# Performance work log

Measured on AMD Instinct MI355X. Metric: run time of the kernel, lower is better.

Reference implementation:

```python
import jax, jax.numpy as jnp
import numpy as np

D_MODEL = 1024
NUM_HEADS = 16
D_K = D_MODEL // NUM_HEADS
D_FF = 4096
B, S = 4, 2048
EPS = 1e-5


def _linear_params(key, d_in, d_out):
    # torch nn.Linear default init: U(-1/sqrt(d_in), 1/sqrt(d_in))
    k1, k2 = jax.random.split(key)
    bound = 1.0 / np.sqrt(d_in)
    W = jax.random.uniform(k1, (d_in, d_out), jnp.float32, -bound, bound)
    b = jax.random.uniform(k2, (d_out,), jnp.float32, -bound, bound)
    return W, b


def setup_inputs() -> dict:
    key = jax.random.key(0)
    ks = jax.random.split(key, 8)
    x = jax.random.normal(ks[0], (B, S, D_MODEL), jnp.float32)
    Wq, bq = _linear_params(ks[1], D_MODEL, D_MODEL)
    Wk, bk = _linear_params(ks[2], D_MODEL, D_MODEL)
    Wv, bv = _linear_params(ks[3], D_MODEL, D_MODEL)
    Wo, bo = _linear_params(ks[4], D_MODEL, D_MODEL)
    W1, b1 = _linear_params(ks[5], D_MODEL, D_FF)
    W2, b2 = _linear_params(ks[6], D_FF, D_MODEL)
    ln1_g = jnp.ones((D_MODEL,), jnp.float32)
    ln1_b = jnp.zeros((D_MODEL,), jnp.float32)
    ln2_g = jnp.ones((D_MODEL,), jnp.float32)
    ln2_b = jnp.zeros((D_MODEL,), jnp.float32)
    return dict(x=x, Wq=Wq, bq=bq, Wk=Wk, bk=bk, Wv=Wv, bv=bv, Wo=Wo, bo=bo,
                W1=W1, b1=b1, W2=W2, b2=b2,
                ln1_g=ln1_g, ln1_b=ln1_b, ln2_g=ln2_g, ln2_b=ln2_b)


def _layernorm(x, g, b):
    mu = jnp.mean(x, axis=-1, keepdims=True)
    var = jnp.mean(jnp.square(x - mu), axis=-1, keepdims=True)
    return (x - mu) * jax.lax.rsqrt(var + EPS) * g + b


def _attention(h, Wq, bq, Wk, bk, Wv, bv, Wo, bo):
    b, s, _ = h.shape
    def split_heads(t):  # (b,s,d) -> (b,H,s,dk)
        return t.reshape(b, s, NUM_HEADS, D_K).transpose(0, 2, 1, 3)
    Q = split_heads(h @ Wq + bq)
    K = split_heads(h @ Wk + bk)
    V = split_heads(h @ Wv + bv)
    scores = jnp.einsum('bhqd,bhkd->bhqk', Q, K) / np.sqrt(D_K)
    causal = jnp.tril(jnp.ones((s, s), dtype=bool))  # True = keep
    scores = jnp.where(causal, scores, -jnp.inf)
    attn = jax.nn.softmax(scores, axis=-1)
    out = jnp.einsum('bhqk,bhkd->bhqd', attn, V)
    out = out.transpose(0, 2, 1, 3).reshape(b, s, D_MODEL)
    return out @ Wo + bo


def reference(x, Wq, bq, Wk, bk, Wv, bv, Wo, bo, W1, b1, W2, b2,
              ln1_g, ln1_b, ln2_g, ln2_b):
    # pre-norm residual block
    x = x + _attention(_layernorm(x, ln1_g, ln1_b), Wq, bq, Wk, bk, Wv, bv, Wo, bo)
    h = _layernorm(x, ln2_g, ln2_b)
    x = x + (jax.nn.relu(h @ W1 + b1) @ W2 + b2)
    return x
```

## Files before the change

### kernel.cpp

```cpp
#include <hip/hip_runtime.h>
#include <hip/hip_bf16.h>

typedef __bf16 bf16;
typedef __attribute__((ext_vector_type(8))) __bf16 bf16x8;
typedef __attribute__((ext_vector_type(4))) float f32x4;

#define D_MODEL 1024
#define NHEADS  16
#define DK      64
#define DFF     4096
#define BATCH   4
#define SEQ     2048
#define NTOK    (BATCH*SEQ)
#define QSCALE  0.18033688011112042f

__device__ __forceinline__ void gload16(const bf16* g, bf16* l) {
    __builtin_amdgcn_global_load_lds((const __attribute__((address_space(1))) void*)g,
                                     (__attribute__((address_space(3))) void*)l, 16, 0, 0);
}

__global__ __launch_bounds__(256) void transpose_cast4(
    const float* __restrict__ W0, const float* __restrict__ W1,
    const float* __restrict__ W2, const float* __restrict__ W3,
    bf16* __restrict__ T0, bf16* __restrict__ T1,
    bf16* __restrict__ T2, bf16* __restrict__ T3)
{
    const int z = blockIdx.z;
    const float* W = (z == 0) ? W0 : (z == 1) ? W1 : (z == 2) ? W2 : W3;
    bf16*       Wt = (z == 0) ? T0 : (z == 1) ? T1 : (z == 2) ? T2 : T3;
    const int K = 1024, N = 1024;
    __shared__ float tile[32][33];
    const int tx = threadIdx.x, ty = threadIdx.y;
    const int n0 = blockIdx.x * 32, k0 = blockIdx.y * 32;
#pragma unroll
    for (int i = 0; i < 4; ++i)
        tile[ty + i*8][tx] = W[(size_t)(k0 + ty + i*8) * N + n0 + tx];
    __syncthreads();
#pragma unroll
    for (int i = 0; i < 4; ++i)
        Wt[(size_t)(n0 + ty + i*8) * K + k0 + tx] = (bf16)tile[tx][ty + i*8];
}

__global__ __launch_bounds__(256) void transpose_cast(
    const float* __restrict__ W, bf16* __restrict__ Wt, int K, int N)
{
    __shared__ float tile[32][33];
    const int tx = threadIdx.x, ty = threadIdx.y;
    const int n0 = blockIdx.x * 32, k0 = blockIdx.y * 32;
#pragma unroll
    for (int i = 0; i < 4; ++i)
        tile[ty + i*8][tx] = W[(size_t)(k0 + ty + i*8) * N + n0 + tx];
    __syncthreads();
#pragma unroll
    for (int i = 0; i < 4; ++i)
        Wt[(size_t)(n0 + ty + i*8) * K + k0 + tx] = (bf16)tile[tx][ty + i*8];
}

__global__ __launch_bounds__(256) void transpose_v(
    const bf16* __restrict__ V, bf16* __restrict__ VT)
{
    __shared__ bf16 t[64][72];
    const int bh = blockIdx.y;
    const int s0 = blockIdx.x * 64;
    const int r  = threadIdx.x >> 2;
    const int c0 = (threadIdx.x & 3) * 16;
    const bf16* Vb = V  + (size_t)bh * SEQ * DK;
    bf16*       Tb = VT + (size_t)bh * DK * SEQ;
#pragma unroll
    for (int i = 0; i < 2; ++i) {
        bf16x8 v = *(const bf16x8*)&Vb[(size_t)(s0 + r) * DK + c0 + i*8];
#pragma unroll
        for (int j = 0; j < 8; ++j) t[c0 + i*8 + j][r] = v[j];
    }
    __syncthreads();
#pragma unroll
    for (int i = 0; i < 2; ++i) {
        bf16x8 o;
#pragma unroll
        for (int j = 0; j < 8; ++j) o[j] = t[r][c0 + i*8 + j];
        *(bf16x8*)&Tb[(size_t)r * SEQ + s0 + c0 + i*8] = o;
    }
}

__global__ __launch_bounds__(256) void ln_kernel(
    const float* __restrict__ x, const float* __restrict__ g,
    const float* __restrict__ beta, bf16* __restrict__ out)
{
    const int row = blockIdx.x, tid = threadIdx.x;
    const f32x4* xr = (const f32x4*)(x + (size_t)row * D_MODEL);
    f32x4 v = xr[tid];
    float s  = v[0] + v[1] + v[2] + v[3];
    float s2 = v[0]*v[0] + v[1]*v[1] + v[2]*v[2] + v[3]*v[3];
#pragma unroll
    for (int off = 32; off > 0; off >>= 1) {
        s  += __shfl_down(s,  off, 64);
        s2 += __shfl_down(s2, off, 64);
    }
    __shared__ float red[8];
    const int wave = tid >> 6, lane = tid & 63;
    if (lane == 0) { red[wave] = s; red[wave + 4] = s2; }
    __syncthreads();
    if (tid == 0) {
        float a = red[0] + red[1] + red[2] + red[3];
        float c = red[4] + red[5] + red[6] + red[7];
        float mu  = a * (1.0f / D_MODEL);
        float var = c * (1.0f / D_MODEL) - mu * mu;
        red[0] = mu;
        red[1] = rsqrtf(var + 1e-5f);
    }
    __syncthreads();
    const float mu = red[0], rs = red[1];
    f32x4 gv = ((const f32x4*)g)[tid];
    f32x4 bv = ((const f32x4*)beta)[tid];
    union { bf16 h[4]; uint2 u; } o;
#pragma unroll
    for (int i = 0; i < 4; ++i) o.h[i] = (bf16)((v[i] - mu) * rs * gv[i] + bv[i]);
    *(uint2*)(out + (size_t)row * D_MODEL + tid * 4) = o.u;
}

template<int EPI>
__global__ __launch_bounds__(256, 2) void gemm_bf16(
    const bf16* __restrict__ A, const bf16* __restrict__ Bt,
    const float* __restrict__ bias, const float* __restrict__ bias2,
    const float* __restrict__ bias3, const float* __restrict__ resid,
    void* __restrict__ outp, int M, int N, int K)
{
    __shared__ __align__(16) bf16 As[128 * 32];
    __shared__ __align__(16) bf16 Bs[128 * 32];
    const int tid  = threadIdx.x;
    const int wave = tid >> 6, lane = tid & 63;
    const int quad = lane >> 4, l16 = lane & 15;
    const int wr = wave >> 1, wc = wave & 1;
    const int m0 = blockIdx.x * 128, n0 = blockIdx.y * 128;

    const int r0 = wave * 32 + (lane >> 2);
    const int r1 = r0 + 16;
    const int u0 = ((lane & 3) - ((r0 >> 1) & 3)) & 3;
    const int u1 = ((lane & 3) - ((r1 >> 1) & 3)) & 3;
    const bf16* gA0 = A  + (size_t)(m0 + r0) * K + u0 * 8;
    const bf16* gA1 = A  + (size_t)(m0 + r1) * K + u1 * 8;
    const bf16* gB0 = Bt + (size_t)(n0 + r0) * K + u0 * 8;
    const bf16* gB1 = Bt + (size_t)(n0 + r1) * K + u1 * 8;
    bf16* lA0 = As + wave * 1024;
    bf16* lA1 = As + wave * 1024 + 512;
    bf16* lB0 = Bs + wave * 1024;
    bf16* lB1 = Bs + wave * 1024 + 512;

    int aoff[4], boff[4];
#pragma unroll
    for (int i = 0; i < 4; ++i) {
        const int ra = wr * 64 + i * 16 + l16;
        aoff[i] = ra * 32 + ((quad + ((ra >> 1) & 3)) & 3) * 8;
        const int rb = wc * 64 + i * 16 + l16;
        boff[i] = rb * 32 + ((quad + ((rb >> 1) & 3)) & 3) * 8;
    }

    const f32x4 vzero = {0.f, 0.f, 0.f, 0.f};
    f32x4 acc[4][4];
#pragma unroll
    for (int i = 0; i < 4; ++i)
#pragma unroll
        for (int j = 0; j < 4; ++j) acc[i][j] = vzero;

    for (int k0 = 0; k0 < K; k0 += 32) {
        __syncthreads();
        gload16(gA0 + k0, lA0);
        gload16(gA1 + k0, lA1);
        gload16(gB0 + k0, lB0);
        gload16(gB1 + k0, lB1);
        __syncthreads();
        bf16x8 af[4], bfr[4];
#pragma unroll
        for (int i = 0; i < 4; ++i) af[i]  = *(const bf16x8*)&As[aoff[i]];
#pragma unroll
        for (int j = 0; j < 4; ++j) bfr[j] = *(const bf16x8*)&Bs[boff[j]];
#pragma unroll
        for (int i = 0; i < 4; ++i)
#pragma unroll
            for (int j = 0; j < 4; ++j)
                acc[i][j] = __builtin_amdgcn_mfma_f32_16x16x32_bf16(af[i], bfr[j], acc[i][j], 0, 0, 0);
    }

#pragma unroll
    for (int i = 0; i < 4; ++i) {
#pragma unroll
        for (int j = 0; j < 4; ++j) {
            const int col = n0 + wc * 64 + j * 16 + l16;
            float bcol, sc = 1.0f;
            if (EPI == 0) {
                const int seg = col >> 10;
                const float* bp = (seg == 0) ? bias : ((seg == 1) ? bias2 : bias3);
                bcol = bp[col & 1023];
                if (seg == 0) sc = QSCALE;
            } else {
                bcol = bias[col];
            }
#pragma unroll
            for (int r = 0; r < 4; ++r) {
                const int row = m0 + wr * 64 + i * 16 + quad * 4 + r;
                const float v = acc[i][j][r] + bcol;
                if (EPI == 0) {
                    const int bb = row >> 11, ss = row & (SEQ - 1);
                    const int hh = (col & 1023) >> 6, dd = col & (DK - 1);
                    const size_t seg = (size_t)(col >> 10);
                    ((bf16*)outp)[seg * 8388608 + (((size_t)(bb * NHEADS + hh)) * SEQ + ss) * DK + dd] = (bf16)(v * sc);
                } else if (EPI == 1) {
                    const size_t idx = (size_t)row * N + col;
                    ((float*)outp)[idx] = v + resid[idx];
                } else {
                    ((bf16*)outp)[(size_t)row * N + col] = (bf16)fmaxf(v, 0.f);
                }
            }
        }
    }
}

__global__ __launch_bounds__(256, 3) void attn_kernel(
    const bf16* __restrict__ Q, const bf16* __restrict__ K,
    const bf16* __restrict__ VT, bf16* __restrict__ out)
{
    const int bh = blockIdx.x;
    const int qt = 15 - (int)blockIdx.y;
    const int b = bh >> 4, h = bh & 15;
    const int tid  = threadIdx.x;
    const int wave = tid >> 6, lane = tid & 63;
    const int quad = lane >> 4, l16 = lane & 15;

    __shared__ __align__(16) bf16 smem[8192 + 8192 + 4 * 1280];
    bf16* Ks = smem;
    bf16* Vt = smem + 8192;
    bf16* Pw = smem + 16384 + wave * 1280;

    const bf16* Qb = Q  + (size_t)bh * SEQ * DK;
    const bf16* Kb = K  + (size_t)bh * SEQ * DK;
    const bf16* Vb = VT + (size_t)bh * DK * SEQ;

    int goK[4], goV[4];
    bf16 *lK[4], *lV[4];
#pragma unroll
    for (int i = 0; i < 4; ++i) {
        const int U = (wave * 4 + i) * 64 + lane;
        const int rK = U >> 3, uK = (U & 7) ^ (rK & 7);
        goK[i] = rK * DK + uK * 8;
        lK[i]  = Ks + (wave * 4 + i) * 512;
        const int rV = U >> 4, usw = U & 15;
        const int uV = (usw & 8) | ((usw & 7) ^ (rV & 7));
        goV[i] = rV * SEQ + uV * 8;
        lV[i]  = Vt + (wave * 4 + i) * 512;
    }

    const int qw = qt * 128 + wave * 32;

    bf16x8 qf[2][2];
#pragma unroll
    for (int qi = 0; qi < 2; ++qi)
#pragma unroll
        for (int kk = 0; kk < 2; ++kk)
            qf[qi][kk] = *(const bf16x8*)&Qb[(size_t)(qw + qi*16 + l16) * DK + kk*32 + quad*8];

    const f32x4 vzero = {0.f, 0.f, 0.f, 0.f};
    f32x4 Oacc[2][4];
    float m_[2], l_[2];
#pragma unroll
    for (int qi = 0; qi < 2; ++qi) {
        m_[qi] = -1.0e30f; l_[qi] = 0.f;
#pragma unroll
        for (int dj = 0; dj < 4; ++dj) Oacc[qi][dj] = vzero;
    }

    for (int t = 0; t <= qt; ++t) {
        const int kv0 = t * 128;
        __syncthreads();
#pragma unroll
        for (int i = 0; i < 4; ++i) gload16(Kb + (size_t)kv0 * DK + goK[i], lK[i]);
#pragma unroll
        for (int i = 0; i < 4; ++i) gload16(Vb + kv0 + goV[i], lV[i]);
        __syncthreads();

        f32x4 sv[8][2];
#pragma unroll
        for (int kvt = 0; kvt < 8; ++kvt) {
            const int R = kvt*16 + l16, rx = R & 7;
            bf16x8 kf0 = *(const bf16x8*)&Ks[R*64 + (quad ^ rx)*8];
            bf16x8 kf1 = *(const bf16x8*)&Ks[R*64 + ((quad + 4) ^ rx)*8];
#pragma unroll
            for (int qi = 0; qi < 2; ++qi) {
                f32x4 tacc = vzero;
                tacc = __builtin_amdgcn_mfma_f32_16x16x32_bf16(kf0, qf[qi][0], tacc, 0, 0, 0);
                tacc = __builtin_amdgcn_mfma_f32_16x16x32_bf16(kf1, qf[qi][1], tacc, 0, 0, 0);
                sv[kvt][qi] = tacc;
            }
        }

        if (t == qt) {
#pragma unroll
            for (int kvt = 0; kvt < 8; ++kvt)
#pragma unroll
                for (int qi = 0; qi < 2; ++qi)
#pragma unroll
                    for (int r = 0; r < 4; ++r) {
                        const int kv = kv0 + kvt*16 + quad*4 + r;
                        const int q  = qw + qi*16 + l16;
                        if (kv > q) sv[kvt][qi][r] = -1.0e30f;
                    }
        }

#pragma unroll
        for (int qi = 0; qi < 2; ++qi) {
            float mx = sv[0][qi][0];
#pragma unroll
            for (int kvt = 0; kvt < 8; ++kvt)
#pragma unroll
                for (int r = 0; r < 4; ++r) mx = fmaxf(mx, sv[kvt][qi][r]);
            mx = fmaxf(mx, __shfl_xor(mx, 16, 64));
            mx = fmaxf(mx, __shfl_xor(mx, 32, 64));
            const float newm  = fmaxf(m_[qi], mx);
            const float alpha = exp2f(m_[qi] - newm);
            m_[qi] = newm;
            float rs = 0.f;
#pragma unroll
            for (int kvt = 0; kvt < 8; ++kvt)
#pragma unroll
                for (int r = 0; r < 4; ++r) {
                    const float p = exp2f(sv[kvt][qi][r] - newm);
                    sv[kvt][qi][r] = p;
                    rs += p;
                }
            rs += __shfl_xor(rs, 16, 64);
            rs += __shfl_xor(rs, 32, 64);
            l_[qi] = l_[qi] * alpha + rs;
#pragma unroll
            for (int dj = 0; dj < 4; ++dj) Oacc[qi][dj] *= alpha;
        }

#pragma unroll
        for (int c2 = 0; c2 < 4; ++c2) {
#pragma unroll
            for (int qi = 0; qi < 2; ++qi)
#pragma unroll
                for (int kl = 0; kl < 2; ++kl) {
                    union { bf16 h[4]; unsigned long long u; } pk;
                    const f32x4 s = sv[c2*2 + kl][qi];
#pragma unroll
                    for (int r = 0; r < 4; ++r) pk.h[r] = (bf16)s[r];
                    *(unsigned long long*)&Pw[(qi*16 + l16)*40 + kl*16 + quad*4] = pk.u;
                }
            bf16x8 vf[4];
#pragma unroll
            for (int dj = 0; dj < 4; ++dj) {
                const int R = dj*16 + l16;
                const int u = c2*4 + quad;
                const int usw = (u & 8) | ((u & 7) ^ (R & 7));
                vf[dj] = *(const bf16x8*)&Vt[R*128 + usw*8];
            }
#pragma unroll
            for (int qi = 0; qi < 2; ++qi) {
                bf16x8 pf = *(const bf16x8*)&Pw[(qi*16 + l16)*40 + quad*8];
#pragma unroll
                for (int dj = 0; dj < 4; ++dj)
                    Oacc[qi][dj] = __builtin_amdgcn_mfma_f32_16x16x32_bf16(vf[dj], pf, Oacc[qi][dj], 0, 0, 0);
            }
        }
    }

    __syncthreads();
    bf16* Ow = smem + wave * 2304;
#pragma unroll
    for (int qi = 0; qi < 2; ++qi) {
        const float inv = 1.0f / l_[qi];
#pragma unroll
        for (int dj = 0; dj < 4; ++dj) {
            union { bf16 h[4]; unsigned long long u; } ok;
#pragma unroll
            for (int r = 0; r < 4; ++r) ok.h[r] = (bf16)(Oacc[qi][dj][r] * inv);
            *(unsigned long long*)&Ow[(qi*16 + l16)*72 + dj*16 + quad*4] = ok.u;
        }
    }
    const int rl = lane >> 3, ul = lane & 7;
#pragma unroll
    for (int i = 0; i < 4; ++i) {
        const int row = rl + i*8;
        const int q = qw + row;
        bf16x8 o = *(const bf16x8*)&Ow[row*72 + ul*8];
        *(bf16x8*)&out[((size_t)(b*SEQ + q))*D_MODEL + h*DK + ul*8] = o;
    }
}

extern "C" void kernel_launch(void* const* d_in, const int* in_sizes, int n_in,
                              void* d_out, int out_size, void* d_ws, size_t ws_size,
                              hipStream_t stream)
{
    const float* x    = (const float*)d_in[0];
    const float* Wq   = (const float*)d_in[1];
    const float* bq   = (const float*)d_in[2];
    const float* Wk   = (const float*)d_in[3];
    const float* bk   = (const float*)d_in[4];
    const float* Wv   = (const float*)d_in[5];
    const float* bv   = (const float*)d_in[6];
    const float* Wo   = (const float*)d_in[7];
    const float* bo   = (const float*)d_in[8];
    const float* W1   = (const float*)d_in[9];
    const float* b1   = (const float*)d_in[10];
    const float* W2   = (const float*)d_in[11];
    const float* b2   = (const float*)d_in[12];
    const float* ln1g = (const float*)d_in[13];
    const float* ln1b = (const float*)d_in[14];
    const float* ln2g = (const float*)d_in[15];
    const float* ln2b = (const float*)d_in[16];

    char* ws = (char*)d_ws;
    const size_t MB = 1024 * 1024;
    bf16* WTq  = (bf16*)(ws + 0 * MB);
    bf16* WTk  = (bf16*)(ws + 2 * MB);
    bf16* WTv  = (bf16*)(ws + 4 * MB);
    bf16* WTo  = (bf16*)(ws + 6 * MB);
    bf16* WT1  = (bf16*)(ws + 8 * MB);
    bf16* WT2  = (bf16*)(ws + 16 * MB);
    bf16* hbuf = (bf16*)(ws + 24 * MB);
    bf16* VhT  = (bf16*)(ws + 24 * MB);
    bf16* Qh   = (bf16*)(ws + 40 * MB);
    bf16* Kh   = (bf16*)(ws + 56 * MB);
    bf16* Vh   = (bf16*)(ws + 72 * MB);
    bf16* attn = (bf16*)(ws + 88 * MB);
    bf16* ff1  = (bf16*)(ws + 40 * MB);
    float* x2  = (float*)d_out;

    dim3 tb(32, 8);
    transpose_cast4<<<dim3(32, 32, 4), tb, 0, stream>>>(Wq, Wk, Wv, Wo, WTq, WTk, WTv, WTo);
    transpose_cast<<<dim3(128, 32), tb, 0, stream>>>(W1, WT1, 1024, 4096);
    transpose_cast<<<dim3(32, 128), tb, 0, stream>>>(W2, WT2, 4096, 1024);

    ln_kernel<<<NTOK, 256, 0, stream>>>(x, ln1g, ln1b, hbuf);

    gemm_bf16<0><<<dim3(64, 24), 256, 0, stream>>>(hbuf, WTq, bq, bk, bv, nullptr, Qh, NTOK, 3072, 1024);

    transpose_v<<<dim3(32, 64), 256, 0, stream>>>(Vh, VhT);

    attn_kernel<<<dim3(64, 16), 256, 0, stream>>>(Qh, Kh, VhT, attn);

    gemm_bf16<1><<<dim3(64, 8), 256, 0, stream>>>(attn, WTo, bo, nullptr, nullptr, x, x2, NTOK, 1024, 1024);

    ln_kernel<<<NTOK, 256, 0, stream>>>(x2, ln2g, ln2b, hbuf);

    gemm_bf16<2><<<dim3(64, 32), 256, 0, stream>>>(hbuf, WT1, b1, nullptr, nullptr, nullptr, ff1, NTOK, 4096, 1024);
    gemm_bf16<1><<<dim3(64, 8),  256, 0, stream>>>(ff1, WT2, b2, nullptr, nullptr, x2, x2, NTOK, 1024, 4096);
}
```

Measured before the change: 531.7 us.

## Pair causal query tiles per block and double-buffer K/V loads in attention

Each attention block now processes two query tiles (one long and one short causal row) so every block does equal work, and the grid is halved. K/V tiles are double-buffered in shared memory, so the next tile's global-to-LDS load is issued before computing on the current one, and the first tile of the second phase is prefetched during the first. Shared memory grows and the occupancy hint drops from 3 to 2 blocks per CU. The output is staged through the per-wave P buffer in halves.

```diff
diff --git a/kernel.cpp b/kernel.cpp
--- a/kernel.cpp
+++ b/kernel.cpp
@@ -215,174 +215,188 @@
     }
 }
 
-__global__ __launch_bounds__(256, 3) void attn_kernel(
+__global__ __launch_bounds__(256, 2) void attn_kernel(
     const bf16* __restrict__ Q, const bf16* __restrict__ K,
     const bf16* __restrict__ VT, bf16* __restrict__ out)
 {
     const int bh = blockIdx.x;
-    const int qt = 15 - (int)blockIdx.y;
     const int b = bh >> 4, h = bh & 15;
     const int tid  = threadIdx.x;
     const int wave = tid >> 6, lane = tid & 63;
     const int quad = lane >> 4, l16 = lane & 15;
 
-    __shared__ __align__(16) bf16 smem[8192 + 8192 + 4 * 1280];
-    bf16* Ks = smem;
-    bf16* Vt = smem + 8192;
-    bf16* Pw = smem + 16384 + wave * 1280;
+    __shared__ __align__(16) bf16 smem[32768 + 4 * 1152];
+    bf16* Pw = smem + 32768 + wave * 1152;
 
     const bf16* Qb = Q  + (size_t)bh * SEQ * DK;
     const bf16* Kb = K  + (size_t)bh * SEQ * DK;
     const bf16* Vb = VT + (size_t)bh * DK * SEQ;
 
-    int goK[4], goV[4];
-    bf16 *lK[4], *lV[4];
+    int goK[4], goV[4], lo[4];
 #pragma unroll
     for (int i = 0; i < 4; ++i) {
         const int U = (wave * 4 + i) * 64 + lane;
         const int rK = U >> 3, uK = (U & 7) ^ (rK & 7);
         goK[i] = rK * DK + uK * 8;
-        lK[i]  = Ks + (wave * 4 + i) * 512;
         const int rV = U >> 4, usw = U & 15;
         const int uV = (usw & 8) | ((usw & 7) ^ (rV & 7));
         goV[i] = rV * SEQ + uV * 8;
-        lV[i]  = Vt + (wave * 4 + i) * 512;
-    }
-
-    const int qw = qt * 128 + wave * 32;
-
-    bf16x8 qf[2][2];
-#pragma unroll
-    for (int qi = 0; qi < 2; ++qi)
-#pragma unroll
-        for (int kk = 0; kk < 2; ++kk)
-            qf[qi][kk] = *(const bf16x8*)&Qb[(size_t)(qw + qi*16 + l16) * DK + kk*32 + quad*8];
+        lo[i]  = (wave * 4 + i) * 512;
+    }
+
+    auto stage = [&](int buf, int t) {
+        const bf16* kp = Kb + (size_t)(t * 128) * DK;
+        const bf16* vp = Vb + t * 128;
+        bf16* kb = smem + buf * 8192;
+        bf16* vb = smem + 16384 + buf * 8192;
+#pragma unroll
+        for (int i = 0; i < 4; ++i) gload16(kp + goK[i], kb + lo[i]);
+#pragma unroll
+        for (int i = 0; i < 4; ++i) gload16(vp + goV[i], vb + lo[i]);
+    };
 
     const f32x4 vzero = {0.f, 0.f, 0.f, 0.f};
-    f32x4 Oacc[2][4];
-    float m_[2], l_[2];
-#pragma unroll
-    for (int qi = 0; qi < 2; ++qi) {
-        m_[qi] = -1.0e30f; l_[qi] = 0.f;
-#pragma unroll
-        for (int dj = 0; dj < 4; ++dj) Oacc[qi][dj] = vzero;
-    }
-
-    for (int t = 0; t <= qt; ++t) {
-        const int kv0 = t * 128;
-        __syncthreads();
-#pragma unroll
-        for (int i = 0; i < 4; ++i) gload16(Kb + (size_t)kv0 * DK + goK[i], lK[i]);
-#pragma unroll
-        for (int i = 0; i < 4; ++i) gload16(Vb + kv0 + goV[i], lV[i]);
-        __syncthreads();
-
-        f32x4 sv[8][2];
-#pragma unroll
-        for (int kvt = 0; kvt < 8; ++kvt) {
-            const int R = kvt*16 + l16, rx = R & 7;
-            bf16x8 kf0 = *(const bf16x8*)&Ks[R*64 + (quad ^ rx)*8];
-            bf16x8 kf1 = *(const bf16x8*)&Ks[R*64 + ((quad + 4) ^ rx)*8];
+    int g = 0;
+    stage(0, 0);
+
+    for (int phase = 0; phase < 2; ++phase) {
+        const int qt = phase ? (int)blockIdx.y : 15 - (int)blockIdx.y;
+        const int qw = qt * 128 + wave * 32;
+
+        bf16x8 qf[2][2];
+#pragma unroll
+        for (int qi = 0; qi < 2; ++qi)
+#pragma unroll
+            for (int kk = 0; kk < 2; ++kk)
+                qf[qi][kk] = *(const bf16x8*)&Qb[(size_t)(qw + qi*16 + l16) * DK + kk*32 + quad*8];
+
+        f32x4 Oacc[2][4];
+        float m_[2], l_[2];
+#pragma unroll
+        for (int qi = 0; qi < 2; ++qi) {
+            m_[qi] = -1.0e30f; l_[qi] = 0.f;
+#pragma unroll
+            for (int dj = 0; dj < 4; ++dj) Oacc[qi][dj] = vzero;
+        }
+
+        for (int t = 0; t <= qt; ++t, ++g) {
+            const int cur = g & 1;
+            __syncthreads();
+            if (t < qt)            stage(cur ^ 1, t + 1);
+            else if (phase == 0)   stage(cur ^ 1, 0);
+            const bf16* kb = smem + cur * 8192;
+            const bf16* vb = smem + 16384 + cur * 8192;
+            const int kv0 = t * 128;
+
+            f32x4 sv[8][2];
+#pragma unroll
+            for (int kvt = 0; kvt < 8; ++kvt) {
+                const int R = kvt*16 + l16, rx = R & 7;
+                bf16x8 kf0 = *(const bf16x8*)&kb[R*64 + (quad ^ rx)*8];
+                bf16x8 kf1 = *(const bf16x8*)&kb[R*64 + (((quad + 4) & 7) ^ rx)*8];
+#pragma unroll
+                for (int qi = 0; qi < 2; ++qi) {
+                    f32x4 tacc = vzero;
+                    tacc = __builtin_amdgcn_mfma_f32_16x16x32_bf16(kf0, qf[qi][0], tacc, 0, 0, 0);
+                    tacc = __builtin_amdgcn_mfma_f32_16x16x32_bf16(kf1, qf[qi][1], tacc, 0, 0, 0);
+                    sv[kvt][qi] = tacc;
+                }
+            }
+
+            if (t == qt) {
+#pragma unroll
+                for (int kvt = 0; kvt < 8; ++kvt)
+#pragma unroll
+                    for (int qi = 0; qi < 2; ++qi)
+#pragma unroll
+                        for (int r = 0; r < 4; ++r) {
+                            const int kv = kv0 + kvt*16 + quad*4 + r;
+                            const int q  = qw + qi*16 + l16;
+                            if (kv > q) sv[kvt][qi][r] = -1.0e30f;
+                        }
+            }
+
 #pragma unroll
             for (int qi = 0; qi < 2; ++qi) {
-                f32x4 tacc = vzero;
-                tacc = __builtin_amdgcn_mfma_f32_16x16x32_bf16(kf0, qf[qi][0], tacc, 0, 0, 0);
-                tacc = __builtin_amdgcn_mfma_f32_16x16x32_bf16(kf1, qf[qi][1], tacc, 0, 0, 0);
-                sv[kvt][qi] = tacc;
+                float mx = sv[0][qi][0];
+#pragma unroll
+                for (int kvt = 0; kvt < 8; ++kvt)
+#pragma unroll
+                    for (int r = 0; r < 4; ++r) mx = fmaxf(mx, sv[kvt][qi][r]);
+                mx = fmaxf(mx, __shfl_xor(mx, 16, 64));
+                mx = fmaxf(mx, __shfl_xor(mx, 32, 64));
+                const float newm  = fmaxf(m_[qi], mx);
+                const float alpha = exp2f(m_[qi] - newm);
+                m_[qi] = newm;
+                float rs = 0.f;
+#pragma unroll
+                for (int kvt = 0; kvt < 8; ++kvt)
+#pragma unroll
+                    for (int r = 0; r < 4; ++r) {
+                        const float p = exp2f(sv[kvt][qi][r] - newm);
+                        sv[kvt][qi][r] = p;
+                        rs += p;
+                    }
+                rs += __shfl_xor(rs, 16, 64);
+                rs += __shfl_xor(rs, 32, 64);
+                l_[qi] = l_[qi] * alpha + rs;
+#pragma unroll
+                for (int dj = 0; dj < 4; ++dj) Oacc[qi][dj] *= alpha;
+            }
+
+#pragma unroll
+            for (int c2 = 0; c2 < 4; ++c2) {
+#pragma unroll
+                for (int qi = 0; qi < 2; ++qi)
+#pragma unroll
+                    for (int kl = 0; kl < 2; ++kl) {
+                        union { bf16 h[4]; unsigned long long u; } pk;
+                        const f32x4 s = sv[c2*2 + kl][qi];
+#pragma unroll
+                        for (int r = 0; r < 4; ++r) pk.h[r] = (bf16)s[r];
+                        *(unsigned long long*)&Pw[(qi*16 + l16)*36 + kl*16 + quad*4] = pk.u;
+                    }
+                bf16x8 vf[4];
+#pragma unroll
+                for (int dj = 0; dj < 4; ++dj) {
+                    const int R = dj*16 + l16;
+                    const int u = c2*4 + quad;
+                    const int usw = (u & 8) | ((u & 7) ^ (R & 7));
+                    vf[dj] = *(const bf16x8*)&vb[R*128 + usw*8];
+                }
+#pragma unroll
+                for (int qi = 0; qi < 2; ++qi) {
+                    bf16x8 pf = *(const bf16x8*)&Pw[(qi*16 + l16)*36 + quad*8];
+#pragma unroll
+                    for (int dj = 0; dj < 4; ++dj)
+                        Oacc[qi][dj] = __builtin_amdgcn_mfma_f32_16x16x32_bf16(vf[dj], pf, Oacc[qi][dj], 0, 0, 0);
+                }
             }
         }
 
-        if (t == qt) {
-#pragma unroll
-            for (int kvt = 0; kvt < 8; ++kvt)
-#pragma unroll
-                for (int qi = 0; qi < 2; ++qi)
-#pragma unroll
-                    for (int r = 0; r < 4; ++r) {
-                        const int kv = kv0 + kvt*16 + quad*4 + r;
-                        const int q  = qw + qi*16 + l16;
-                        if (kv > q) sv[kvt][qi][r] = -1.0e30f;
-                    }
+        const float inv0 = 1.0f / l_[0], inv1 = 1.0f / l_[1];
+#pragma unroll
+        for (int dh = 0; dh < 2; ++dh) {
+#pragma unroll
+            for (int qi = 0; qi < 2; ++qi) {
+                const float inv = qi ? inv1 : inv0;
+#pragma unroll
+                for (int djl = 0; djl < 2; ++djl) {
+                    const int dj = dh*2 + djl;
+                    union { bf16 h[4]; unsigned long long u; } ok;
+#pragma unroll
+                    for (int r = 0; r < 4; ++r) ok.h[r] = (bf16)(Oacc[qi][dj][r] * inv);
+                    *(unsigned long long*)&Pw[(qi*16 + l16)*36 + djl*16 + quad*4] = ok.u;
+                }
+            }
+            const int row = lane >> 1;
+#pragma unroll
+            for (int it = 0; it < 2; ++it) {
+                const int grp = (lane & 1) + 2*it;
+                bf16x8 o = *(const bf16x8*)&Pw[row*36 + grp*8];
+                *(bf16x8*)&out[((size_t)(b*SEQ + qw - wave*32 + wave*32 + row))*D_MODEL + h*DK + dh*32 + grp*8] = o;
+            }
         }
-
-#pragma unroll
-        for (int qi = 0; qi < 2; ++qi) {
-            float mx = sv[0][qi][0];
-#pragma unroll
-            for (int kvt = 0; kvt < 8; ++kvt)
-#pragma unroll
-                for (int r = 0; r < 4; ++r) mx = fmaxf(mx, sv[kvt][qi][r]);
-            mx = fmaxf(mx, __shfl_xor(mx, 16, 64));
-            mx = fmaxf(mx, __shfl_xor(mx, 32, 64));
-            const float newm  = fmaxf(m_[qi], mx);
-            const float alpha = exp2f(m_[qi] - newm);
-            m_[qi] = newm;
-            float rs = 0.f;
-#pragma unroll
-            for (int kvt = 0; kvt < 8; ++kvt)
-#pragma unroll
-                for (int r = 0; r < 4; ++r) {
-                    const float p = exp2f(sv[kvt][qi][r] - newm);
-                    sv[kvt][qi][r] = p;
-                    rs += p;
-                }
-            rs += __shfl_xor(rs, 16, 64);
-            rs += __shfl_xor(rs, 32, 64);
-            l_[qi] = l_[qi] * alpha + rs;
-#pragma unroll
-            for (int dj = 0; dj < 4; ++dj) Oacc[qi][dj] *= alpha;
-        }
-
-#pragma unroll
-        for (int c2 = 0; c2 < 4; ++c2) {
-#pragma unroll
-            for (int qi = 0; qi < 2; ++qi)
-#pragma unroll
-                for (int kl = 0; kl < 2; ++kl) {
-                    union { bf16 h[4]; unsigned long long u; } pk;
-                    const f32x4 s = sv[c2*2 + kl][qi];
-#pragma unroll
-                    for (int r = 0; r < 4; ++r) pk.h[r] = (bf16)s[r];
-                    *(unsigned long long*)&Pw[(qi*16 + l16)*40 + kl*16 + quad*4] = pk.u;
-                }
-            bf16x8 vf[4];
-#pragma unroll
-            for (int dj = 0; dj < 4; ++dj) {
-                const int R = dj*16 + l16;
-                const int u = c2*4 + quad;
-                const int usw = (u & 8) | ((u & 7) ^ (R & 7));
-                vf[dj] = *(const bf16x8*)&Vt[R*128 + usw*8];
-            }
-#pragma unroll
-            for (int qi = 0; qi < 2; ++qi) {
-                bf16x8 pf = *(const bf16x8*)&Pw[(qi*16 + l16)*40 + quad*8];
-#pragma unroll
-                for (int dj = 0; dj < 4; ++dj)
-                    Oacc[qi][dj] = __builtin_amdgcn_mfma_f32_16x16x32_bf16(vf[dj], pf, Oacc[qi][dj], 0, 0, 0);
-            }
-        }
-    }
-
-    __syncthreads();
-    bf16* Ow = smem + wave * 2304;
-#pragma unroll
-    for (int qi = 0; qi < 2; ++qi) {
-        const float inv = 1.0f / l_[qi];
-#pragma unroll
-        for (int dj = 0; dj < 4; ++dj) {
-            union { bf16 h[4]; unsigned long long u; } ok;
-#pragma unroll
-            for (int r = 0; r < 4; ++r) ok.h[r] = (bf16)(Oacc[qi][dj][r] * inv);
-            *(unsigned long long*)&Ow[(qi*16 + l16)*72 + dj*16 + quad*4] = ok.u;
-        }
-    }
-    const int rl = lane >> 3, ul = lane & 7;
-#pragma unroll
-    for (int i = 0; i < 4; ++i) {
-        const int row = rl + i*8;
-        const int q = qw + row;
-        bf16x8 o = *(const bf16x8*)&Ow[row*72 + ul*8];
-        *(bf16x8*)&out[((size_t)(b*SEQ + q))*D_MODEL + h*DK + ul*8] = o;
     }
 }
 
@@ -436,7 +450,7 @@
 
     transpose_v<<<dim3(32, 64), 256, 0, stream>>>(Vh, VhT);
 
-    attn_kernel<<<dim3(64, 16), 256, 0, stream>>>(Qh, Kh, VhT, attn);
+    attn_kernel<<<dim3(64, 8), 256, 0, stream>>>(Qh, Kh, VhT, attn);
 
     gemm_bf16<1><<<dim3(64, 8), 256, 0, stream>>>(attn, WTo, bo, nullptr, nullptr, x, x2, NTOK, 1024, 1024);
 
```

Result: faster. 519.2 us (-2.4%).
